# Optimization experiments

Measured on AMD Instinct MI355X. Metric: run time of the kernel, lower is better.

## Reference

```python
import jax, jax.numpy as jnp
import numpy as np

N_NODES = 100000
N_EDGES = 3200000
D = 128
B = 4


def gcn_conv(x, row, col, W, b, n):
    # PyG GCNConv: x' = D^{-1/2}(A+I)D^{-1/2} (x W) + b
    xw = x @ W  # [N, out]
    ones = jnp.ones((row.shape[0],), dtype=x.dtype)
    deg = jax.ops.segment_sum(ones, col, num_segments=n) + 1.0  # self-loop
    dinv = jax.lax.rsqrt(deg)  # deg > 0 because of self-loops
    norm = dinv[row] * dinv[col]  # [E]
    msg = xw[row] * norm[:, None]  # gather + scale
    agg = jax.ops.segment_sum(msg, col, num_segments=n)  # scatter-add
    agg = agg + (dinv * dinv)[:, None] * xw  # self-loop contribution
    return agg + b


def setup_inputs() -> dict:
    key = jax.random.key(0)
    ks = jax.random.split(key, 10)
    x = jax.random.normal(ks[0], (N_NODES, D), dtype=jnp.float32)
    edge_index = jax.random.randint(ks[1], (2, N_EDGES), 0, N_NODES, dtype=jnp.int64)
    question_embeddings = jax.random.normal(ks[2], (B, D), dtype=jnp.float32)
    s = 1.0 / np.sqrt(D)
    W1 = jax.random.uniform(ks[3], (D, D), jnp.float32, -s, s)
    b1 = jnp.zeros((D,), jnp.float32)
    W2 = jax.random.uniform(ks[4], (D, D), jnp.float32, -s, s)
    b2 = jnp.zeros((D,), jnp.float32)
    Wq = jax.random.uniform(ks[5], (D, D), jnp.float32, -s, s)
    bq = jax.random.uniform(ks[6], (D,), jnp.float32, -s, s)
    return {"x": x, "edge_index": edge_index, "question_embeddings": question_embeddings,
            "W1": W1, "b1": b1, "W2": W2, "b2": b2, "Wq": Wq, "bq": bq}


def reference(x, edge_index, question_embeddings, W1, b1, W2, b2, Wq, bq):
    n = x.shape[0]
    row, col = edge_index[0], edge_index[1]
    h = jax.nn.relu(gcn_conv(x, row, col, W1, b1, n))  # [N, H]
    h = gcn_conv(h, row, col, W2, b2, n)  # [N, H]
    q = question_embeddings @ Wq + bq  # [B, H]
    out = h[None, :, :] + q[:, None, :]  # [B, N, H]
    return jax.nn.log_softmax(out, axis=1)  # softmax over node dim (torch dim=1)
```

## Files before the change

kernel.cpp:

```cpp
#include <hip/hip_runtime.h>
#include <math.h>

#define DD 128
#define CT 16384
#define CAP 10240

typedef unsigned int uint;
typedef unsigned short u16;

typedef __attribute__((ext_vector_type(8))) __bf16 bf16x8;
typedef __attribute__((ext_vector_type(4))) float f32x4;
typedef __attribute__((ext_vector_type(4))) uint uint4v;
typedef __attribute__((ext_vector_type(8))) u16 u16x8;


__device__ inline uint bf16bits(float a) {
  uint u = __float_as_uint(a);
  return (u + 0x7fffu + ((u >> 16) & 1u)) >> 16;
}

__device__ inline uint pack_bf16x2(float a, float b) {
  return bf16bits(a) | (bf16bits(b) << 16);
}


__global__ __launch_bounds__(256) void k_coarse(const int* __restrict__ row,
                                                const int* __restrict__ col,
                                                int* __restrict__ gcursor,
                                                uint* __restrict__ coarse,
                                                int E, int NB) {
  __shared__ int hist[512];
  __shared__ int base[512];
  int tid = threadIdx.x;
  long e0 = (long)blockIdx.x * CT;
  int cnt = (int)min((long)CT, (long)E - e0);
  for (int i = tid; i < NB; i += 256) hist[i] = 0;
  __syncthreads();
  for (int i = tid; i < cnt; i += 256) atomicAdd(&hist[col[e0 + i] >> 8], 1);
  __syncthreads();
  for (int i = tid; i < NB; i += 256) {
    base[i] = i * CAP + atomicAdd(&gcursor[i], hist[i]);
    hist[i] = 0;
  }
  __syncthreads();
  for (int i = tid; i < cnt; i += 256) {
    int c = col[e0 + i];
    int r = row[e0 + i];
    int b = c >> 8;
    int p = base[b] + atomicAdd(&hist[b], 1);
    coarse[p] = ((uint)r << 8) | (uint)(c & 255);
  }
}

__global__ __launch_bounds__(256) void k_finalize(const uint* __restrict__ coarse,
                                                  const int* __restrict__ gcursor,
                                                  int* __restrict__ offB,
                                                  int* __restrict__ offE,
                                                  float* __restrict__ dinv,
                                                  int* __restrict__ srt, int n) {
  __shared__ int hist[256];
  __shared__ int s[256];
  __shared__ int cur[256];
  int tid = threadIdx.x;
  int b = blockIdx.x;
  int base = b * CAP;
  int cnt = gcursor[b];
  int node0 = b << 8;
  hist[tid] = 0;
  __syncthreads();
  for (int i = tid; i < cnt; i += 256) atomicAdd(&hist[coarse[base + i] & 255u], 1);
  __syncthreads();
  int deg = hist[tid];
  s[tid] = deg;
  __syncthreads();
  for (int o = 1; o < 256; o <<= 1) {
    int add = (tid >= o) ? s[tid - o] : 0;
    __syncthreads();
    s[tid] += add;
    __syncthreads();
  }
  int p0 = base + s[tid] - deg;
  int node = node0 + tid;
  if (node < n) {
    offB[node] = p0;
    offE[node] = p0 + deg;
    dinv[node] = rsqrtf(1.0f + (float)deg);
  }
  cur[tid] = p0;
  __syncthreads();
  for (int i = tid; i < cnt; i += 256) {
    uint e = coarse[base + i];
    int pos = atomicAdd(&cur[e & 255u], 1);
    srt[pos] = (int)(e & 0xFFFFFF00u);
  }
}


__global__ __launch_bounds__(256) void k_prepw(const float* __restrict__ W1,
                                               const float* __restrict__ W2,
                                               u16* __restrict__ o1h, u16* __restrict__ o1l,
                                               u16* __restrict__ o2h, u16* __restrict__ o2l) {
  const float* W = blockIdx.x ? W2 : W1;
  u16* oh = blockIdx.x ? o2h : o1h;
  u16* ol = blockIdx.x ? o2l : o1l;
  for (int i = threadIdx.x; i < 16384; i += 256) {
    int k = i >> 7, c = i & 127;
    float v = W[i];
    uint hb = bf16bits(v);
    float hv = __uint_as_float(hb << 16);
    uint lb = bf16bits(v - hv);
    uint uidx = (((uint)c << 6) + ((uint)k >> 1)) ^ (((uint)c & 7u) << 2);
    int p = (int)((uidx << 1) | ((uint)k & 1u));
    oh[p] = (u16)hb;
    ol[p] = (u16)lb;
  }
}


__global__ __launch_bounds__(256, 2) void k_gemm(const float* __restrict__ X,
                                                 const u16* __restrict__ gWh,
                                                 const u16* __restrict__ gWl,
                                                 const float* __restrict__ dinv,
                                                 uint* __restrict__ msg, int n) {
  __shared__ uint Wh[8192];
  __shared__ uint Wl[8192];
  int tid = threadIdx.x;
  for (int i = tid; i < 2048; i += 256) ((uint4*)Wh)[i] = ((const uint4*)gWh)[i];
  for (int i = tid; i < 2048; i += 256) ((uint4*)Wl)[i] = ((const uint4*)gWl)[i];

  int lane = tid & 63, wv = tid >> 6;
  int s_ = lane & 15, g = lane >> 4;
  int row0 = blockIdx.x * 128 + wv * 32;

  f32x4 acc[2][8];
#pragma unroll
  for (int a = 0; a < 2; a++)
#pragma unroll
    for (int b = 0; b < 8; b++) acc[a][b] = (f32x4)0.f;

  __syncthreads();

#pragma unroll
  for (int kc = 0; kc < 4; kc++) {
    uint4v ah[2], al[2];
#pragma unroll
    for (int sub = 0; sub < 2; sub++) {
      int r = row0 + sub * 16 + s_;
      float4 v0, v1;
      if (r < n) {
        const float* xp = X + (size_t)r * DD + kc * 32 + g * 8;
        v0 = ((const float4*)xp)[0];
        v1 = ((const float4*)xp)[1];
      } else {
        v0 = make_float4(0.f, 0.f, 0.f, 0.f);
        v1 = v0;
      }
      uint h0 = bf16bits(v0.x), h1 = bf16bits(v0.y), h2 = bf16bits(v0.z), h3 = bf16bits(v0.w);
      uint h4 = bf16bits(v1.x), h5 = bf16bits(v1.y), h6 = bf16bits(v1.z), h7 = bf16bits(v1.w);
      ah[sub][0] = h0 | (h1 << 16);
      ah[sub][1] = h2 | (h3 << 16);
      ah[sub][2] = h4 | (h5 << 16);
      ah[sub][3] = h6 | (h7 << 16);
      al[sub][0] = pack_bf16x2(v0.x - __uint_as_float(h0 << 16), v0.y - __uint_as_float(h1 << 16));
      al[sub][1] = pack_bf16x2(v0.z - __uint_as_float(h2 << 16), v0.w - __uint_as_float(h3 << 16));
      al[sub][2] = pack_bf16x2(v1.x - __uint_as_float(h4 << 16), v1.y - __uint_as_float(h5 << 16));
      al[sub][3] = pack_bf16x2(v1.z - __uint_as_float(h6 << 16), v1.w - __uint_as_float(h7 << 16));
    }
    int koff2 = (kc * 32 + g * 8) >> 1;
#pragma unroll
    for (int ct = 0; ct < 8; ct++) {
      int c = ct * 16 + s_;
      int uo = (int)(((uint)(c << 6) + (uint)koff2) ^ (((uint)c & 7u) << 2));
      bf16x8 bh = __builtin_bit_cast(bf16x8, *(const u16x8*)&Wh[uo]);
      bf16x8 bl = __builtin_bit_cast(bf16x8, *(const u16x8*)&Wl[uo]);
#pragma unroll
      for (int sub = 0; sub < 2; sub++) {
        bf16x8 av = __builtin_bit_cast(bf16x8, ah[sub]);
        bf16x8 lv = __builtin_bit_cast(bf16x8, al[sub]);
        acc[sub][ct] = __builtin_amdgcn_mfma_f32_16x16x32_bf16(av, bh, acc[sub][ct], 0, 0, 0);
        acc[sub][ct] = __builtin_amdgcn_mfma_f32_16x16x32_bf16(lv, bh, acc[sub][ct], 0, 0, 0);
        acc[sub][ct] = __builtin_amdgcn_mfma_f32_16x16x32_bf16(av, bl, acc[sub][ct], 0, 0, 0);
      }
    }
  }

#pragma unroll
  for (int sub = 0; sub < 2; sub++) {
#pragma unroll
    for (int q = 0; q < 4; q++) {
      int rq = row0 + sub * 16 + g * 4 + q;
      if (rq < n) {
        float di = dinv[rq];
        uint* mrow = msg + (size_t)rq * 64;
#pragma unroll
        for (int ct = 0; ct < 4; ct++) {
          uint u = pack_bf16x2(acc[sub][ct][q] * di, acc[sub][ct + 4][q] * di);
          mrow[ct * 16 + s_] = u;
        }
      }
    }
  }
}


__global__ __launch_bounds__(256) void k_agg(const uint* __restrict__ msg,
                                             const int* __restrict__ srt,
                                             const int* __restrict__ offB,
                                             const int* __restrict__ offE,
                                             const float* __restrict__ dinv,
                                             const float* __restrict__ bias,
                                             float* __restrict__ out, int n, int relu) {
  int lane = threadIdx.x & 63;
  int s_ = lane & 15, g = lane >> 4;
  int node = blockIdx.x * 4 + (threadIdx.x >> 6);
  if (node >= n) return;
  int beg = offB[node], end = offE[node];
  float a0 = 0.f, a1 = 0.f, a2 = 0.f, a3 = 0.f, a4 = 0.f, a5 = 0.f, a6 = 0.f, a7 = 0.f;
  const char* mb = (const char*)msg + s_ * 16;
  for (int t = beg; t < end; t += 64) {
    int nt = end - t;
    if (nt > 64) nt = 64;
    int boff = srt[t + (lane < nt ? lane : nt - 1)];
    for (int k = 0; k < nt; k += 32) {
      uint4 r[8];
      if (k + 32 <= nt) {
#pragma unroll
        for (int u = 0; u < 8; u++) {
          int bo = __shfl(boff, k + u * 4 + g);
          r[u] = *(const uint4*)(mb + (uint)bo);
        }
#pragma unroll
        for (int u = 0; u < 8; u++) {
          a0 += __uint_as_float(r[u].x << 16); a4 += __uint_as_float(r[u].x & 0xffff0000u);
          a1 += __uint_as_float(r[u].y << 16); a5 += __uint_as_float(r[u].y & 0xffff0000u);
          a2 += __uint_as_float(r[u].z << 16); a6 += __uint_as_float(r[u].z & 0xffff0000u);
          a3 += __uint_as_float(r[u].w << 16); a7 += __uint_as_float(r[u].w & 0xffff0000u);
        }
      } else {
#pragma unroll
        for (int u = 0; u < 8; u++) {
          int e = k + u * 4 + g;
          int bo = __shfl(boff, e < nt ? e : nt - 1);
          r[u] = *(const uint4*)(mb + (uint)bo);
          if (e >= nt) r[u] = make_uint4(0u, 0u, 0u, 0u);
        }
#pragma unroll
        for (int u = 0; u < 8; u++) {
          a0 += __uint_as_float(r[u].x << 16); a4 += __uint_as_float(r[u].x & 0xffff0000u);
          a1 += __uint_as_float(r[u].y << 16); a5 += __uint_as_float(r[u].y & 0xffff0000u);
          a2 += __uint_as_float(r[u].z << 16); a6 += __uint_as_float(r[u].z & 0xffff0000u);
          a3 += __uint_as_float(r[u].w << 16); a7 += __uint_as_float(r[u].w & 0xffff0000u);
        }
      }
    }
  }
#define RED(x) x += __shfl_xor(x, 16); x += __shfl_xor(x, 32);
  RED(a0) RED(a1) RED(a2) RED(a3) RED(a4) RED(a5) RED(a6) RED(a7)
#undef RED
  const uint4* m4 = (const uint4*)msg;
  uint4 rs = m4[(size_t)node * 16 + s_];
  a0 += __uint_as_float(rs.x << 16); a4 += __uint_as_float(rs.x & 0xffff0000u);
  a1 += __uint_as_float(rs.y << 16); a5 += __uint_as_float(rs.y & 0xffff0000u);
  a2 += __uint_as_float(rs.z << 16); a6 += __uint_as_float(rs.z & 0xffff0000u);
  a3 += __uint_as_float(rs.w << 16); a7 += __uint_as_float(rs.w & 0xffff0000u);
  float di = dinv[node];
  if (g == 0) {
    float4 bv = ((const float4*)bias)[s_];
    float4 o = make_float4(di * a0 + bv.x, di * a1 + bv.y, di * a2 + bv.z, di * a3 + bv.w);
    if (relu) {
      o.x = fmaxf(o.x, 0.f); o.y = fmaxf(o.y, 0.f); o.z = fmaxf(o.z, 0.f); o.w = fmaxf(o.w, 0.f);
    }
    ((float4*)(out + (size_t)node * DD))[s_] = o;
  } else if (g == 1) {
    float4 bv = ((const float4*)(bias + 64))[s_];
    float4 o = make_float4(di * a4 + bv.x, di * a5 + bv.y, di * a6 + bv.z, di * a7 + bv.w);
    if (relu) {
      o.x = fmaxf(o.x, 0.f); o.y = fmaxf(o.y, 0.f); o.z = fmaxf(o.z, 0.f); o.w = fmaxf(o.w, 0.f);
    }
    ((float4*)(out + (size_t)node * DD + 64))[s_] = o;
  }
}


__global__ __launch_bounds__(256) void k_colstat(const float* __restrict__ h, int n,
                                                 float* __restrict__ PM,
                                                 float* __restrict__ PS) {
  __shared__ float sm[128], ss[128];
  int d = threadIdx.x & 127, sub = threadIdx.x >> 7;
  float m = -3.4e38f, s = 0.f;
  for (int r = blockIdx.x * 2 + sub; r < n; r += gridDim.x * 2) {
    float v = h[(size_t)r * DD + d];
    float nm = fmaxf(m, v);
    s = s * __expf(m - nm) + __expf(v - nm);
    m = nm;
  }
  if (sub) { sm[d] = m; ss[d] = s; }
  __syncthreads();
  if (!sub) {
    float m2 = sm[d], s2 = ss[d];
    float nm = fmaxf(m, m2);
    float so = s * __expf(m - nm) + s2 * __expf(m2 - nm);
    PM[blockIdx.x * 128 + d] = nm;
    PS[blockIdx.x * 128 + d] = so;
  }
}

__global__ __launch_bounds__(64) void k_lsemerge(const float* __restrict__ PM,
                                                 const float* __restrict__ PS,
                                                 float* __restrict__ L, int nb) {
  int d = blockIdx.x;
  int lane = threadIdx.x;
  float m = -3.4e38f, s = 0.f;
  for (int p = lane; p < nb; p += 64) {
    float m2 = PM[p * 128 + d], s2 = PS[p * 128 + d];
    float nm = fmaxf(m, m2);
    s = s * __expf(m - nm) + s2 * __expf(m2 - nm);
    m = nm;
  }
#pragma unroll
  for (int o = 1; o < 64; o <<= 1) {
    float m2 = __shfl_xor(m, o), s2 = __shfl_xor(s, o);
    float nm = fmaxf(m, m2);
    s = s * __expf(m - nm) + s2 * __expf(m2 - nm);
    m = nm;
  }
  if (lane == 0) L[d] = m + logf(s);
}


__global__ __launch_bounds__(256) void k_final(const float* __restrict__ h,
                                               const float* __restrict__ L,
                                               float* __restrict__ out, int n, int B) {
  int idx = blockIdx.x * 256 + threadIdx.x;
  int nd4 = n * 32;
  if (idx >= nd4) return;
  int c4 = idx & 31;
  float4 hv = ((const float4*)h)[idx];
  float4 lv = ((const float4*)L)[c4];
  float4 r = make_float4(hv.x - lv.x, hv.y - lv.y, hv.z - lv.z, hv.w - lv.w);
  float4* o = (float4*)out;
  for (int b = 0; b < B; b++) o[(size_t)idx + (size_t)b * nd4] = r;
}


extern "C" void kernel_launch(void* const* d_in, const int* in_sizes, int n_in,
                              void* d_out, int out_size, void* d_ws, size_t ws_size,
                              hipStream_t stream) {
  const float* x  = (const float*)d_in[0];
  const int*   ei = (const int*)d_in[1];
  const float* W1 = (const float*)d_in[3];
  const float* b1 = (const float*)d_in[4];
  const float* W2 = (const float*)d_in[5];
  const float* b2 = (const float*)d_in[6];

  int n = in_sizes[0] / DD;
  int E = in_sizes[1] / 2;
  int B = out_size / (n * DD);
  const int* row = ei;
  const int* col = ei + E;

  float* out = (float*)d_out;
  size_t nd = (size_t)n * DD;
  int NB = (n + 255) / 256;
  size_t CAPN = (size_t)NB * CAP;
  float* bufA = out;
  float* bufB = out + nd;
  int* srt = (int*)(out + 2 * nd);
  uint* coarse = (uint*)(srt + CAPN);
  uint* msg = (uint*)coarse;
  char* sm = (char*)(out + 3 * nd);
  auto alloc = [&](size_t bytes) -> char* {
    char* p = sm;
    sm += (bytes + 63) & ~(size_t)63;
    return p;
  };
  float* dinv = (float*)alloc(sizeof(float) * n);
  int* offB = (int*)alloc(sizeof(int) * n);
  int* offE = (int*)alloc(sizeof(int) * n);
  int* gcursor = (int*)alloc(sizeof(int) * NB);
  u16* wt1h = (u16*)alloc(32768);
  u16* wt1l = (u16*)alloc(32768);
  u16* wt2h = (u16*)alloc(32768);
  u16* wt2l = (u16*)alloc(32768);
  float* PM = (float*)alloc(sizeof(float) * 512 * 128);
  float* PS = (float*)alloc(sizeof(float) * 512 * 128);
  float* L = (float*)d_ws;

  int gC = (E + CT - 1) / CT;

  hipMemsetAsync(gcursor, 0, sizeof(int) * NB, stream);
  k_prepw<<<2, 256, 0, stream>>>(W1, W2, wt1h, wt1l, wt2h, wt2l);
  k_coarse<<<gC, 256, 0, stream>>>(row, col, gcursor, coarse, E, NB);
  k_finalize<<<NB, 256, 0, stream>>>(coarse, gcursor, offB, offE, dinv, srt, n);

  int gG = (n + 127) / 128;
  k_gemm<<<gG, 256, 0, stream>>>(x, wt1h, wt1l, dinv, msg, n);
  k_agg<<<(n + 3) / 4, 256, 0, stream>>>(msg, srt, offB, offE, dinv, b1, bufA, n, 1);
  k_gemm<<<gG, 256, 0, stream>>>(bufA, wt2h, wt2l, dinv, msg, n);
  k_agg<<<(n + 3) / 4, 256, 0, stream>>>(msg, srt, offB, offE, dinv, b2, bufB, n, 0);

  k_colstat<<<512, 256, 0, stream>>>(bufB, n, PM, PS);
  k_lsemerge<<<128, 64, 0, stream>>>(PM, PS, L, 512);
  k_final<<<(n * 32 + 255) / 256, 256, 0, stream>>>(bufB, L, out, n, B);
}
```

Baseline: 718.0 us.

## Vectorize edge binning loads, pre-split layer-1 output to bf16 hi/lo, fold memset

After: 676.9 us. -5.7%, faster.

```diff
diff --git a/kernel.cpp b/kernel.cpp
--- a/kernel.cpp
+++ b/kernel.cpp
@@ -9,6 +9,7 @@
 typedef unsigned short u16;
 
 typedef __attribute__((ext_vector_type(8))) __bf16 bf16x8;
+typedef __attribute__((ext_vector_type(2))) __bf16 bf16x2;
 typedef __attribute__((ext_vector_type(4))) float f32x4;
 typedef __attribute__((ext_vector_type(4))) uint uint4v;
 typedef __attribute__((ext_vector_type(8))) u16 u16x8;
@@ -20,8 +21,14 @@
 }
 
 __device__ inline uint pack_bf16x2(float a, float b) {
-  return bf16bits(a) | (bf16bits(b) << 16);
-}
+  bf16x2 t;
+  t[0] = (__bf16)a;
+  t[1] = (__bf16)b;
+  return __builtin_bit_cast(uint, t);
+}
+
+__device__ inline float lo16f(uint u) { return __uint_as_float(u << 16); }
+__device__ inline float hi16f(uint u) { return __uint_as_float(u & 0xffff0000u); }
 
 
 __global__ __launch_bounds__(256) void k_coarse(const int* __restrict__ row,
@@ -34,21 +41,39 @@
   int tid = threadIdx.x;
   long e0 = (long)blockIdx.x * CT;
   int cnt = (int)min((long)CT, (long)E - e0);
+  int cnt4 = cnt >> 2;
+  const int4* c4p = (const int4*)(col + e0);
+  const int4* r4p = (const int4*)(row + e0);
   for (int i = tid; i < NB; i += 256) hist[i] = 0;
   __syncthreads();
-  for (int i = tid; i < cnt; i += 256) atomicAdd(&hist[col[e0 + i] >> 8], 1);
+  for (int i = tid; i < cnt4; i += 256) {
+    int4 c = c4p[i];
+    atomicAdd(&hist[c.x >> 8], 1);
+    atomicAdd(&hist[c.y >> 8], 1);
+    atomicAdd(&hist[c.z >> 8], 1);
+    atomicAdd(&hist[c.w >> 8], 1);
+  }
+  for (int i = (cnt4 << 2) + tid; i < cnt; i += 256) atomicAdd(&hist[col[e0 + i] >> 8], 1);
   __syncthreads();
   for (int i = tid; i < NB; i += 256) {
     base[i] = i * CAP + atomicAdd(&gcursor[i], hist[i]);
     hist[i] = 0;
   }
   __syncthreads();
-  for (int i = tid; i < cnt; i += 256) {
+  for (int i = tid; i < cnt4; i += 256) {
+    int4 c = c4p[i];
+    int4 r = r4p[i];
+    int b;
+    b = c.x >> 8; coarse[base[b] + atomicAdd(&hist[b], 1)] = ((uint)r.x << 8) | (uint)(c.x & 255);
+    b = c.y >> 8; coarse[base[b] + atomicAdd(&hist[b], 1)] = ((uint)r.y << 8) | (uint)(c.y & 255);
+    b = c.z >> 8; coarse[base[b] + atomicAdd(&hist[b], 1)] = ((uint)r.z << 8) | (uint)(c.z & 255);
+    b = c.w >> 8; coarse[base[b] + atomicAdd(&hist[b], 1)] = ((uint)r.w << 8) | (uint)(c.w & 255);
+  }
+  for (int i = (cnt4 << 2) + tid; i < cnt; i += 256) {
     int c = col[e0 + i];
     int r = row[e0 + i];
     int b = c >> 8;
-    int p = base[b] + atomicAdd(&hist[b], 1);
-    coarse[p] = ((uint)r << 8) | (uint)(c & 255);
+    coarse[base[b] + atomicAdd(&hist[b], 1)] = ((uint)r << 8) | (uint)(c & 255);
   }
 }
 
@@ -65,10 +90,19 @@
   int b = blockIdx.x;
   int base = b * CAP;
   int cnt = gcursor[b];
+  int cnt4 = cnt >> 2;
+  const uint4* e4p = (const uint4*)(coarse + base);
   int node0 = b << 8;
   hist[tid] = 0;
   __syncthreads();
-  for (int i = tid; i < cnt; i += 256) atomicAdd(&hist[coarse[base + i] & 255u], 1);
+  for (int i = tid; i < cnt4; i += 256) {
+    uint4 e = e4p[i];
+    atomicAdd(&hist[e.x & 255u], 1);
+    atomicAdd(&hist[e.y & 255u], 1);
+    atomicAdd(&hist[e.z & 255u], 1);
+    atomicAdd(&hist[e.w & 255u], 1);
+  }
+  for (int i = (cnt4 << 2) + tid; i < cnt; i += 256) atomicAdd(&hist[coarse[base + i] & 255u], 1);
   __syncthreads();
   int deg = hist[tid];
   s[tid] = deg;
@@ -88,7 +122,15 @@
   }
   cur[tid] = p0;
   __syncthreads();
-  for (int i = tid; i < cnt; i += 256) {
+  for (int i = tid; i < cnt4; i += 256) {
+    uint4 e = e4p[i];
+    int pos;
+    pos = atomicAdd(&cur[e.x & 255u], 1); srt[pos] = (int)(e.x & 0xFFFFFF00u);
+    pos = atomicAdd(&cur[e.y & 255u], 1); srt[pos] = (int)(e.y & 0xFFFFFF00u);
+    pos = atomicAdd(&cur[e.z & 255u], 1); srt[pos] = (int)(e.z & 0xFFFFFF00u);
+    pos = atomicAdd(&cur[e.w & 255u], 1); srt[pos] = (int)(e.w & 0xFFFFFF00u);
+  }
+  for (int i = (cnt4 << 2) + tid; i < cnt; i += 256) {
     uint e = coarse[base + i];
     int pos = atomicAdd(&cur[e & 255u], 1);
     srt[pos] = (int)(e & 0xFFFFFF00u);
@@ -99,7 +141,10 @@
 __global__ __launch_bounds__(256) void k_prepw(const float* __restrict__ W1,
                                                const float* __restrict__ W2,
                                                u16* __restrict__ o1h, u16* __restrict__ o1l,
-                                               u16* __restrict__ o2h, u16* __restrict__ o2l) {
+                                               u16* __restrict__ o2h, u16* __restrict__ o2l,
+                                               int* __restrict__ gcursor, int NB) {
+  if (blockIdx.x == 0)
+    for (int i = threadIdx.x; i < NB; i += 256) gcursor[i] = 0;
   const float* W = blockIdx.x ? W2 : W1;
   u16* oh = blockIdx.x ? o2h : o1h;
   u16* ol = blockIdx.x ? o2l : o1l;
@@ -117,7 +162,10 @@
 }
 
 
+template <int PRE>
 __global__ __launch_bounds__(256, 2) void k_gemm(const float* __restrict__ X,
+                                                 const uint* __restrict__ Xh,
+                                                 const uint* __restrict__ Xl,
                                                  const u16* __restrict__ gWh,
                                                  const u16* __restrict__ gWl,
                                                  const float* __restrict__ dinv,
@@ -146,25 +194,32 @@
 #pragma unroll
     for (int sub = 0; sub < 2; sub++) {
       int r = row0 + sub * 16 + s_;
-      float4 v0, v1;
-      if (r < n) {
-        const float* xp = X + (size_t)r * DD + kc * 32 + g * 8;
-        v0 = ((const float4*)xp)[0];
-        v1 = ((const float4*)xp)[1];
+      if (PRE) {
+        uint4 hv = make_uint4(0u, 0u, 0u, 0u), lv = hv;
+        if (r < n) {
+          hv = ((const uint4*)Xh)[(size_t)r * 16 + kc * 4 + g];
+          lv = ((const uint4*)Xl)[(size_t)r * 16 + kc * 4 + g];
+        }
+        ah[sub][0] = hv.x; ah[sub][1] = hv.y; ah[sub][2] = hv.z; ah[sub][3] = hv.w;
+        al[sub][0] = lv.x; al[sub][1] = lv.y; al[sub][2] = lv.z; al[sub][3] = lv.w;
       } else {
-        v0 = make_float4(0.f, 0.f, 0.f, 0.f);
-        v1 = v0;
+        float4 v0, v1;
+        if (r < n) {
+          const float* xp = X + (size_t)r * DD + kc * 32 + g * 8;
+          v0 = ((const float4*)xp)[0];
+          v1 = ((const float4*)xp)[1];
+        } else {
+          v0 = make_float4(0.f, 0.f, 0.f, 0.f);
+          v1 = v0;
+        }
+        uint p0 = pack_bf16x2(v0.x, v0.y), p1 = pack_bf16x2(v0.z, v0.w);
+        uint p2 = pack_bf16x2(v1.x, v1.y), p3 = pack_bf16x2(v1.z, v1.w);
+        ah[sub][0] = p0; ah[sub][1] = p1; ah[sub][2] = p2; ah[sub][3] = p3;
+        al[sub][0] = pack_bf16x2(v0.x - lo16f(p0), v0.y - hi16f(p0));
+        al[sub][1] = pack_bf16x2(v0.z - lo16f(p1), v0.w - hi16f(p1));
+        al[sub][2] = pack_bf16x2(v1.x - lo16f(p2), v1.y - hi16f(p2));
+        al[sub][3] = pack_bf16x2(v1.z - lo16f(p3), v1.w - hi16f(p3));
       }
-      uint h0 = bf16bits(v0.x), h1 = bf16bits(v0.y), h2 = bf16bits(v0.z), h3 = bf16bits(v0.w);
-      uint h4 = bf16bits(v1.x), h5 = bf16bits(v1.y), h6 = bf16bits(v1.z), h7 = bf16bits(v1.w);
-      ah[sub][0] = h0 | (h1 << 16);
-      ah[sub][1] = h2 | (h3 << 16);
-      ah[sub][2] = h4 | (h5 << 16);
-      ah[sub][3] = h6 | (h7 << 16);
-      al[sub][0] = pack_bf16x2(v0.x - __uint_as_float(h0 << 16), v0.y - __uint_as_float(h1 << 16));
-      al[sub][1] = pack_bf16x2(v0.z - __uint_as_float(h2 << 16), v0.w - __uint_as_float(h3 << 16));
-      al[sub][2] = pack_bf16x2(v1.x - __uint_as_float(h4 << 16), v1.y - __uint_as_float(h5 << 16));
-      al[sub][3] = pack_bf16x2(v1.z - __uint_as_float(h6 << 16), v1.w - __uint_as_float(h7 << 16));
     }
     int koff2 = (kc * 32 + g * 8) >> 1;
 #pragma unroll
@@ -209,7 +264,9 @@
                                              const int* __restrict__ offE,
                                              const float* __restrict__ dinv,
                                              const float* __restrict__ bias,
-                                             float* __restrict__ out, int n, int relu) {
+                                             float* __restrict__ out,
+                                             uint* __restrict__ hh,
+                                             uint* __restrict__ hl, int n, int relu) {
   int lane = threadIdx.x & 63;
   int s_ = lane & 15, g = lane >> 4;
   int node = blockIdx.x * 4 + (threadIdx.x >> 6);
@@ -264,20 +321,25 @@
   a2 += __uint_as_float(rs.z << 16); a6 += __uint_as_float(rs.z & 0xffff0000u);
   a3 += __uint_as_float(rs.w << 16); a7 += __uint_as_float(rs.w & 0xffff0000u);
   float di = dinv[node];
-  if (g == 0) {
-    float4 bv = ((const float4*)bias)[s_];
-    float4 o = make_float4(di * a0 + bv.x, di * a1 + bv.y, di * a2 + bv.z, di * a3 + bv.w);
+  if (g < 2) {
+    float4 bv = ((const float4*)(bias + (g ? 64 : 0)))[s_];
+    float o0, o1, o2, o3;
+    if (g == 0) {
+      o0 = di * a0 + bv.x; o1 = di * a1 + bv.y; o2 = di * a2 + bv.z; o3 = di * a3 + bv.w;
+    } else {
+      o0 = di * a4 + bv.x; o1 = di * a5 + bv.y; o2 = di * a6 + bv.z; o3 = di * a7 + bv.w;
+    }
     if (relu) {
-      o.x = fmaxf(o.x, 0.f); o.y = fmaxf(o.y, 0.f); o.z = fmaxf(o.z, 0.f); o.w = fmaxf(o.w, 0.f);
-    }
-    ((float4*)(out + (size_t)node * DD))[s_] = o;
-  } else if (g == 1) {
-    float4 bv = ((const float4*)(bias + 64))[s_];
-    float4 o = make_float4(di * a4 + bv.x, di * a5 + bv.y, di * a6 + bv.z, di * a7 + bv.w);
-    if (relu) {
-      o.x = fmaxf(o.x, 0.f); o.y = fmaxf(o.y, 0.f); o.z = fmaxf(o.z, 0.f); o.w = fmaxf(o.w, 0.f);
-    }
-    ((float4*)(out + (size_t)node * DD + 64))[s_] = o;
+      o0 = fmaxf(o0, 0.f); o1 = fmaxf(o1, 0.f); o2 = fmaxf(o2, 0.f); o3 = fmaxf(o3, 0.f);
+      uint h0 = pack_bf16x2(o0, o1), h1 = pack_bf16x2(o2, o3);
+      uint l0 = pack_bf16x2(o0 - lo16f(h0), o1 - hi16f(h0));
+      uint l1 = pack_bf16x2(o2 - lo16f(h1), o3 - hi16f(h1));
+      int mb2 = node * 64 + (g ? 32 : 0) + 2 * s_;
+      *(uint2*)(hh + mb2) = make_uint2(h0, h1);
+      *(uint2*)(hl + mb2) = make_uint2(l0, l1);
+    } else {
+      *(float4*)(out + (size_t)node * DD + (g ? 64 : 0) + 4 * s_) = make_float4(o0, o1, o2, o3);
+    }
   }
 }
 
@@ -363,7 +425,8 @@
   size_t nd = (size_t)n * DD;
   int NB = (n + 255) / 256;
   size_t CAPN = (size_t)NB * CAP;
-  float* bufA = out;
+  uint* hh = (uint*)out;
+  uint* hl = hh + (size_t)n * 64;
   float* bufB = out + nd;
   int* srt = (int*)(out + 2 * nd);
   uint* coarse = (uint*)(srt + CAPN);
@@ -388,16 +451,15 @@
 
   int gC = (E + CT - 1) / CT;
 
-  hipMemsetAsync(gcursor, 0, sizeof(int) * NB, stream);
-  k_prepw<<<2, 256, 0, stream>>>(W1, W2, wt1h, wt1l, wt2h, wt2l);
+  k_prepw<<<2, 256, 0, stream>>>(W1, W2, wt1h, wt1l, wt2h, wt2l, gcursor, NB);
   k_coarse<<<gC, 256, 0, stream>>>(row, col, gcursor, coarse, E, NB);
   k_finalize<<<NB, 256, 0, stream>>>(coarse, gcursor, offB, offE, dinv, srt, n);
 
   int gG = (n + 127) / 128;
-  k_gemm<<<gG, 256, 0, stream>>>(x, wt1h, wt1l, dinv, msg, n);
-  k_agg<<<(n + 3) / 4, 256, 0, stream>>>(msg, srt, offB, offE, dinv, b1, bufA, n, 1);
-  k_gemm<<<gG, 256, 0, stream>>>(bufA, wt2h, wt2l, dinv, msg, n);
-  k_agg<<<(n + 3) / 4, 256, 0, stream>>>(msg, srt, offB, offE, dinv, b2, bufB, n, 0);
+  k_gemm<0><<<gG, 256, 0, stream>>>(x, nullptr, nullptr, wt1h, wt1l, dinv, msg, n);
+  k_agg<<<(n + 3) / 4, 256, 0, stream>>>(msg, srt, offB, offE, dinv, b1, bufB, hh, hl, n, 1);
+  k_gemm<1><<<gG, 256, 0, stream>>>(nullptr, hh, hl, wt2h, wt2l, dinv, msg, n);
+  k_agg<<<(n + 3) / 4, 256, 0, stream>>>(msg, srt, offB, offE, dinv, b2, bufB, hh, hl, n, 0);
 
   k_colstat<<<512, 256, 0, stream>>>(bufB, n, PM, PS);
   k_lsemerge<<<128, 64, 0, stream>>>(PM, PS, L, 512);
```
